# Kernel optimization log

Measured on AMD Instinct MI355X. Metric: run time of the kernel, lower is better.

Reference implementation:

```python
import jax, jax.numpy as jnp
import numpy as np

B, S, E, H = 4, 2048, 1024, 16
D = E // H  # head_dim = 64
SCALE = D ** -0.5
NEG_INF = -1e9


def setup_inputs() -> dict:
    key = jax.random.key(0)
    ks = jax.random.split(key, 12)
    p = 1.0 / np.sqrt(E)  # nn.Linear default init scale
    inp = {
        'query': jax.random.normal(ks[0], (B, S, E), jnp.float32),
        'key': jax.random.normal(ks[1], (B, S, E), jnp.float32),
        'value': jax.random.normal(ks[2], (B, S, E), jnp.float32),
        'mask': jnp.ones((B, S, S), jnp.int32),
        'Wq': jax.random.uniform(ks[3], (E, E), jnp.float32, -p, p),
        'bq': jax.random.uniform(ks[4], (E,), jnp.float32, -p, p),
        'Wk': jax.random.uniform(ks[5], (E, E), jnp.float32, -p, p),
        'bk': jax.random.uniform(ks[6], (E,), jnp.float32, -p, p),
        'Wv': jax.random.uniform(ks[7], (E, E), jnp.float32, -p, p),
        'bv': jax.random.uniform(ks[8], (E,), jnp.float32, -p, p),
        'Wo': jax.random.uniform(ks[9], (E, E), jnp.float32, -p, p),
        'bo': jax.random.uniform(ks[10], (E,), jnp.float32, -p, p),
    }
    return inp


def _heads(x):
    # [B, S, E] -> [B, H, S, D]
    b, s, _ = x.shape
    return x.reshape(b, s, H, D).transpose(0, 2, 1, 3)


def reference(query, key, value, mask, Wq, bq, Wk, bk, Wv, bv, Wo, bo):
    # separate QKV projections (nn.Linear: x @ W.T + b)
    q = _heads(query @ Wq.T + bq) * SCALE  # query pre-scaled as in module
    k = _heads(key @ Wk.T + bk)
    v = _heads(value @ Wv.T + bv)
    # scaled dot-product attention with explicit score matrix
    scores = jnp.einsum('bhqd,bhkd->bhqk', q, k)  # [B, H, S, S]
    m = mask[:, None, :, :]  # broadcast over heads
    scores = jnp.where(m == 0, NEG_INF, scores)
    attn = jax.nn.softmax(scores, axis=-1)
    out = jnp.einsum('bhqk,bhkd->bhqd', attn, v)  # [B, H, S, D]
    out = out.transpose(0, 2, 1, 3).reshape(query.shape[0], -1, E)
    return out @ Wo.T + bo
```

## Files before the change

### kernel.cpp

```cpp
#include <hip/hip_runtime.h>


#define B_ 4
#define S_ 2048
#define E_ 1024
#define H_ 16
#define D_ 64

typedef __attribute__((ext_vector_type(4))) float f32x4;
typedef __attribute__((ext_vector_type(8))) short short8;
typedef __attribute__((ext_vector_type(4))) short short4v;
typedef __attribute__((ext_vector_type(8))) __bf16 bf16x8;
typedef __attribute__((ext_vector_type(4))) __bf16 bf16x4;
typedef unsigned short u16;
typedef unsigned int u32;

#define MFMA16(A, Bf, C) __builtin_amdgcn_mfma_f32_16x16x32_bf16((A), (Bf), (C), 0, 0, 0)

#define FMAXB2 12.0f

__device__ __forceinline__ f32x4 mfma_pv(short4v a, short4v b, f32x4 c) {
  return __builtin_amdgcn_mfma_f32_16x16x16bf16_1k(a, b, c, 0, 0, 0);
}

__device__ __forceinline__ u16 f2bf(float f) {
  u32 u = __float_as_uint(f);
  u += 0x7FFFu + ((u >> 16) & 1u);
  return (u16)(u >> 16);
}

__device__ __forceinline__ void async16(const void* g, void* l) {
  __builtin_amdgcn_global_load_lds((const __attribute__((address_space(1))) u32*)g,
                                   (__attribute__((address_space(3))) u32*)l, 16, 0, 0);
}

__device__ __forceinline__ short4v packp(float a, float b, float c, float d) {
  bf16x4 t;
  t[0] = (__bf16)a; t[1] = (__bf16)b; t[2] = (__bf16)c; t[3] = (__bf16)d;
  return __builtin_bit_cast(short4v, t);
}

__device__ __forceinline__ float exp2fast(float x) {
  return __builtin_amdgcn_exp2f(x);
}

__global__ __launch_bounds__(256) void cvt8_kernel(const float* __restrict__ a0,
                                                   const float* __restrict__ a1,
                                                   const float* __restrict__ a2,
                                                   const float* __restrict__ w0,
                                                   const float* __restrict__ w1,
                                                   const float* __restrict__ w2,
                                                   const float* __restrict__ w3,
                                                   u16* __restrict__ da0,
                                                   u16* __restrict__ da1,
                                                   u16* __restrict__ da2,
                                                   u16* __restrict__ dw0,
                                                   u16* __restrict__ dw1,
                                                   u16* __restrict__ dw2,
                                                   u16* __restrict__ dw3,
                                                   const int* __restrict__ mask,
                                                   u32* __restrict__ mbits,
                                                   int* __restrict__ rowOK,
                                                   int n4a, int n4w) {
  int z = blockIdx.y;
  if (z == 7) {
    if (blockIdx.x >= 2048) return;
    int w = threadIdx.x >> 6, t = threadIdx.x & 63;
    int row = blockIdx.x * 4 + w;
    const int4* p = (const int4*)(mask + (size_t)row * S_ + t * 32);
    u32 bits = 0;
#pragma unroll
    for (int i = 0; i < 8; ++i) {
      int4 v = p[i];
      bits |= (v.x != 0 ? 1u : 0u) << (i * 4 + 0);
      bits |= (v.y != 0 ? 1u : 0u) << (i * 4 + 1);
      bits |= (v.z != 0 ? 1u : 0u) << (i * 4 + 2);
      bits |= (v.w != 0 ? 1u : 0u) << (i * 4 + 3);
    }
    mbits[(size_t)row * 64 + t] = bits;
    unsigned long long all1 = __ballot(bits == 0xFFFFFFFFu);
    if (t == 0) rowOK[row] = (all1 == 0xFFFFFFFFFFFFFFFFull) ? 1 : 0;
    return;
  }
  const float* src;
  u16* dst;
  int n4;
  switch (z) {
    case 0: src = a0; dst = da0; n4 = n4a; break;
    case 1: src = a1; dst = da1; n4 = n4a; break;
    case 2: src = a2; dst = da2; n4 = n4a; break;
    case 3: src = w0; dst = dw0; n4 = n4w; break;
    case 4: src = w1; dst = dw1; n4 = n4w; break;
    case 5: src = w2; dst = dw2; n4 = n4w; break;
    default: src = w3; dst = dw3; n4 = n4w; break;
  }
  int i = blockIdx.x * 256 + threadIdx.x;
  if (i >= n4) return;
  float4 v = ((const float4*)src)[i];
  short4v o;
  o[0] = (short)f2bf(v.x); o[1] = (short)f2bf(v.y);
  o[2] = (short)f2bf(v.z); o[3] = (short)f2bf(v.w);
  ((short4v*)dst)[i] = o;
}

__device__ __forceinline__ void gemm_swizzle(int* m0, int* n0) {
  int s = blockIdx.y * 8 + blockIdx.x;
  int L = (s & 7) * 64 + (s >> 3);
  *m0 = (L >> 3) * 128;
  *n0 = (L & 7) * 128;
}

__device__ __forceinline__ void gemm_mainloop_128(const u16* __restrict__ A,
                                                  const u16* __restrict__ W,
                                                  int m0, int n0,
                                                  u16* As, u16* Bs,
                                                  f32x4 acc[4][4], int tid) {
  int w = tid >> 6, l = tid & 63, lo = l & 15, g = l >> 4;
  int wm = w >> 1, wn = w & 1;
  int srow = w * 32 + (l >> 3);
  int scol = ((l & 7) ^ (l >> 3)) * 8;
  const u16* ga0 = A + (size_t)(m0 + srow) * E_ + scol;
  const u16* gb0 = W + (size_t)(n0 + srow) * E_ + scol;
  char* la0 = (char*)As + w * 4096;
  char* lb0 = (char*)Bs + w * 4096;

  for (int k0 = 0; k0 < E_; k0 += 64) {
#pragma unroll
    for (int i = 0; i < 4; ++i) {
      async16(ga0 + (size_t)i * 8 * E_ + k0, la0 + i * 1024);
      async16(gb0 + (size_t)i * 8 * E_ + k0, lb0 + i * 1024);
    }
    __syncthreads();
#pragma unroll
    for (int kh = 0; kh < 2; ++kh) {
      bf16x8 af[4], bf[4];
#pragma unroll
      for (int mi = 0; mi < 4; ++mi) {
        int r = wm * 64 + mi * 16 + lo;
        af[mi] = *(const bf16x8*)((char*)As + r * 128 + (((kh * 4 + g) ^ (r & 7)) * 16));
      }
#pragma unroll
      for (int ni = 0; ni < 4; ++ni) {
        int r = wn * 64 + ni * 16 + lo;
        bf[ni] = *(const bf16x8*)((char*)Bs + r * 128 + (((kh * 4 + g) ^ (r & 7)) * 16));
      }
#pragma unroll
      for (int mi = 0; mi < 4; ++mi)
#pragma unroll
        for (int ni = 0; ni < 4; ++ni)
          acc[mi][ni] = MFMA16(af[mi], bf[ni], acc[mi][ni]);
    }
    __syncthreads();
  }
}

__global__ __launch_bounds__(256) void gemm_qkv_kernel(
    const u16* __restrict__ qin, const u16* __restrict__ kin, const u16* __restrict__ vin,
    const u16* __restrict__ wq, const u16* __restrict__ wk, const u16* __restrict__ wv,
    const float* __restrict__ bq, const float* __restrict__ bk, const float* __restrict__ bv,
    u16* __restrict__ Qo, u16* __restrict__ Ko, u16* __restrict__ Vo) {
  __shared__ u16 As[128 * 64];
  __shared__ u16 Bs[128 * 64];
  int z = blockIdx.z;
  const u16* A = z == 0 ? qin : (z == 1 ? kin : vin);
  const u16* W = z == 0 ? wq : (z == 1 ? wk : wv);
  const float* bias = z == 0 ? bq : (z == 1 ? bk : bv);
  u16* O = z == 0 ? Qo : (z == 1 ? Ko : Vo);
  float scale = z == 0 ? 0.125f * 1.44269504f : 1.0f;
  int m0, n0;
  gemm_swizzle(&m0, &n0);
  f32x4 acc[4][4];
#pragma unroll
  for (int mi = 0; mi < 4; ++mi)
#pragma unroll
    for (int ni = 0; ni < 4; ++ni) acc[mi][ni] = (f32x4){0.f, 0.f, 0.f, 0.f};
  int tid = threadIdx.x;
  gemm_mainloop_128(A, W, m0, n0, As, Bs, acc, tid);
  int w = tid >> 6, l = tid & 63, lo = l & 15, g = l >> 4;
  int wm = w >> 1, wn = w & 1;
#pragma unroll
  for (int mi = 0; mi < 4; ++mi)
#pragma unroll
    for (int ni = 0; ni < 4; ++ni) {
      int n = n0 + wn * 64 + ni * 16 + lo;
      int h = n >> 6, d = n & 63;
      float bb = bias[n];
      int mbase = m0 + wm * 64 + mi * 16 + g * 4;
      int b = mbase >> 11, s = mbase & 2047;
      if (z == 2) {
        short4v ov;
#pragma unroll
        for (int j = 0; j < 4; ++j) ov[j] = (short)f2bf(acc[mi][ni][j] + bb);
        *(short4v*)(O + (((size_t)(b * H_ + h)) * D_ + d) * S_ + s) = ov;
      } else {
#pragma unroll
        for (int j = 0; j < 4; ++j) {
          float val = (acc[mi][ni][j] + bb) * scale;
          O[(((size_t)(b * H_ + h)) * S_ + (s + j)) * D_ + d] = f2bf(val);
        }
      }
    }
}

__global__ __launch_bounds__(256) void gemm_out_kernel(const u16* __restrict__ A,
                                                       const u16* __restrict__ W,
                                                       const float* __restrict__ bias,
                                                       float* __restrict__ O) {
  __shared__ u16 As[128 * 64];
  __shared__ u16 Bs[128 * 64];
  int m0, n0;
  gemm_swizzle(&m0, &n0);
  f32x4 acc[4][4];
#pragma unroll
  for (int mi = 0; mi < 4; ++mi)
#pragma unroll
    for (int ni = 0; ni < 4; ++ni) acc[mi][ni] = (f32x4){0.f, 0.f, 0.f, 0.f};
  int tid = threadIdx.x;
  gemm_mainloop_128(A, W, m0, n0, As, Bs, acc, tid);
  int w = tid >> 6, l = tid & 63, lo = l & 15, g = l >> 4;
  int wm = w >> 1, wn = w & 1;
#pragma unroll
  for (int mi = 0; mi < 4; ++mi)
#pragma unroll
    for (int ni = 0; ni < 4; ++ni) {
      int n = n0 + wn * 64 + ni * 16 + lo;
      float bb = bias[n];
#pragma unroll
      for (int j = 0; j < 4; ++j) {
        int m = m0 + wm * 64 + mi * 16 + g * 4 + j;
        O[(size_t)m * E_ + n] = acc[mi][ni][j] + bb;
      }
    }
}

__global__ __launch_bounds__(256) void attn_kernel(const u16* __restrict__ Q,
                                                   const u16* __restrict__ K,
                                                   const u16* __restrict__ VT,
                                                   u16* __restrict__ AO,
                                                   const u32* __restrict__ mbits,
                                                   const int* __restrict__ rowOK) {
  __shared__ u16 Kt0[4096], Kt1[4096];
  __shared__ u16 Vt0[4096], Vt1[4096];
  __shared__ int s_ok;

  int tid = threadIdx.x;
  int w = tid >> 6, l = tid & 63, lo = l & 15, g = l >> 4;
  int flat = blockIdx.y * gridDim.x + blockIdx.x;
  int L = (flat & 7) * 128 + (flat >> 3);
  int bh = L >> 4;
  int b = bh >> 4, h = bh & 15;
  int q0 = (L & 15) * 128;

  if (tid == 0) s_ok = 1;
  __syncthreads();
  if (tid < 128 && rowOK[b * S_ + q0 + tid] == 0) s_ok = 0;
  __syncthreads();
  const bool use_mask = (s_ok == 0);

  const u16* Qb = Q + (size_t)bh * S_ * D_;
  const u16* Kb = K + (size_t)bh * S_ * D_;
  const u16* VTb = VT + (size_t)bh * D_ * S_;

  const u16* kg[2];
  const u16* vgb[2];
  int lbase[2];
#pragma unroll
  for (int r = 0; r < 2; ++r) {
    int kb = r * 4 + w;
    int tr = kb * 8 + (l >> 3);
    int dc = (l & 7) ^ (l >> 3);
    kg[r] = Kb + (size_t)tr * D_ + dc * 8;
    vgb[r] = VTb + (size_t)tr * S_ + dc * 8;
    lbase[r] = kb * 512;
  }
#pragma unroll
  for (int r = 0; r < 2; ++r) {
    async16(kg[r], &Kt0[lbase[r]]);
    async16(vgb[r], &Vt0[lbase[r]]);
  }

  int qrow = q0 + w * 32;
  bf16x8 qf[2][2];
#pragma unroll
  for (int qi = 0; qi < 2; ++qi)
#pragma unroll
    for (int kc = 0; kc < 2; ++kc)
      qf[qi][kc] = *(const bf16x8*)(Qb + (size_t)(qrow + qi * 16 + lo) * D_ + kc * 32 + g * 8);

  f32x4 ot[4][2];
  f32x4 lacc[2];
#pragma unroll
  for (int di = 0; di < 4; ++di)
#pragma unroll
    for (int qi = 0; qi < 2; ++qi) ot[di][qi] = (f32x4){0.f, 0.f, 0.f, 0.f};
  lacc[0] = (f32x4){0.f, 0.f, 0.f, 0.f};
  lacc[1] = (f32x4){0.f, 0.f, 0.f, 0.f};
  float m_run[2] = {-__builtin_inff(), -__builtin_inff()};
  const short4v onesv = {(short)0x3F80, (short)0x3F80, (short)0x3F80, (short)0x3F80};
  const f32x4 cinit = {-FMAXB2, -FMAXB2, -FMAXB2, -FMAXB2};

  auto tile_body = [&](const u16* KtC, const u16* VtC, u16* KtN, u16* VtN, int kk) {
    __syncthreads();
    if (kk + 64 < S_) {
#pragma unroll
      for (int r = 0; r < 2; ++r) {
        async16(kg[r] + (size_t)(kk + 64) * D_, &KtN[lbase[r]]);
        async16(vgb[r] + (kk + 64), &VtN[lbase[r]]);
      }
    }
    const char* Ktc = (const char*)KtC;
    const char* Vtc = (const char*)VtC;

    short4v pb[4][2];
    if (!use_mask) {
      __builtin_amdgcn_s_setprio(1);
#pragma unroll
      for (int ks = 0; ks < 4; ++ks) {
        int row = ks * 16 + lo;
        bf16x8 a0 = *(const bf16x8*)(Ktc + row * 128 + ((g * 16) ^ ((row & 7) << 4)));
        bf16x8 a1 = *(const bf16x8*)(Ktc + row * 128 + ((64 + g * 16) ^ ((row & 7) << 4)));
        f32x4 c0 = MFMA16(a0, qf[0][0], cinit);
        c0 = MFMA16(a1, qf[0][1], c0);
        f32x4 c1 = MFMA16(a0, qf[1][0], cinit);
        c1 = MFMA16(a1, qf[1][1], c1);
        pb[ks][0] = packp(exp2fast(c0[0]), exp2fast(c0[1]), exp2fast(c0[2]),
                          exp2fast(c0[3]));
        pb[ks][1] = packp(exp2fast(c1[0]), exp2fast(c1[1]), exp2fast(c1[2]),
                          exp2fast(c1[3]));
      }
      __builtin_amdgcn_s_setprio(0);
    } else {
      float tmx[2] = {-__builtin_inff(), -__builtin_inff()};
#pragma unroll
      for (int ks = 0; ks < 4; ++ks) {
        int row = ks * 16 + lo;
        bf16x8 a0 = *(const bf16x8*)(Ktc + row * 128 + ((g * 16) ^ ((row & 7) << 4)));
        bf16x8 a1 = *(const bf16x8*)(Ktc + row * 128 + ((64 + g * 16) ^ ((row & 7) << 4)));
#pragma unroll
        for (int qi = 0; qi < 2; ++qi) {
          f32x4 c = MFMA16(a0, qf[qi][0], cinit);
          c = MFMA16(a1, qf[qi][1], c);
          int q = qrow + qi * 16 + lo;
          u32 word = mbits[((size_t)(b * S_ + q)) * 64 + ((kk + ks * 16 + g * 4) >> 5)];
#pragma unroll
          for (int j = 0; j < 4; ++j) {
            int kkk = ks * 16 + g * 4 + j;
            if (!((word >> ((kk + kkk) & 31)) & 1u)) c[j] = -1e9f;
            tmx[qi] = fmaxf(tmx[qi], c[j]);
          }
        }
      }
#pragma unroll
      for (int qi = 0; qi < 2; ++qi) {
        float t = tmx[qi];
        t = fmaxf(t, __shfl_xor(t, 16, 64));
        t = fmaxf(t, __shfl_xor(t, 32, 64));
        float mnew = fmaxf(m_run[qi], t);
        float alpha = exp2fast(m_run[qi] - mnew);
        m_run[qi] = mnew;
#pragma unroll
        for (int di = 0; di < 4; ++di) ot[di][qi] *= alpha;
        lacc[qi] *= alpha;
      }
#pragma unroll
      for (int ks = 0; ks < 4; ++ks) {
        int row = ks * 16 + lo;
        bf16x8 a0 = *(const bf16x8*)(Ktc + row * 128 + ((g * 16) ^ ((row & 7) << 4)));
        bf16x8 a1 = *(const bf16x8*)(Ktc + row * 128 + ((64 + g * 16) ^ ((row & 7) << 4)));
#pragma unroll
        for (int qi = 0; qi < 2; ++qi) {
          f32x4 c = MFMA16(a0, qf[qi][0], cinit);
          c = MFMA16(a1, qf[qi][1], c);
          int q = qrow + qi * 16 + lo;
          u32 word = mbits[((size_t)(b * S_ + q)) * 64 + ((kk + ks * 16 + g * 4) >> 5)];
          float mm = m_run[qi];
#pragma unroll
          for (int j = 0; j < 4; ++j) {
            int kkk = ks * 16 + g * 4 + j;
            if (!((word >> ((kk + kkk) & 31)) & 1u)) c[j] = -1e9f;
            c[j] = exp2fast(c[j] - mm);
          }
          pb[ks][qi] = packp(c[0], c[1], c[2], c[3]);
        }
      }
    }

#pragma unroll
    for (int ks = 0; ks < 4; ++ks)
#pragma unroll
      for (int qi = 0; qi < 2; ++qi)
        lacc[qi] = mfma_pv(onesv, pb[ks][qi], lacc[qi]);

    short4v vaA[4], vaB[4];
#define LOADVA(arr, ksv)                                                              \
  _Pragma("unroll") for (int di = 0; di < 4; ++di) {                                  \
    int r = di * 16 + lo;                                                             \
    int chunk = (ksv)*2 + (g >> 1);                                                   \
    arr[di] = *(const short4v*)(Vtc + r * 128 + (((chunk * 16) ^ ((r & 7) << 4))) +   \
                                ((g & 1) * 8));                                       \
  }
#define MFMAKS(arr, ksv)                                                              \
  _Pragma("unroll") for (int qi = 0; qi < 2; ++qi) {                                  \
    _Pragma("unroll") for (int di = 0; di < 4; ++di)                                  \
        ot[di][qi] = mfma_pv(arr[di], pb[ksv][qi], ot[di][qi]);                       \
  }
    LOADVA(vaA, 0)
    LOADVA(vaB, 1)
    __builtin_amdgcn_s_setprio(1);
    MFMAKS(vaA, 0)
    LOADVA(vaA, 2)
    MFMAKS(vaB, 1)
    LOADVA(vaB, 3)
    MFMAKS(vaA, 2)
    MFMAKS(vaB, 3)
    __builtin_amdgcn_s_setprio(0);
#undef LOADVA
#undef MFMAKS
  };

  for (int k0 = 0; k0 < S_; k0 += 128) {
    tile_body(Kt0, Vt0, Kt1, Vt1, k0);
    tile_body(Kt1, Vt1, Kt0, Vt0, k0 + 64);
  }

#pragma unroll
  for (int qi = 0; qi < 2; ++qi) {
    float inv = 1.f / lacc[qi][0];
    int q = qrow + qi * 16 + lo;
#pragma unroll
    for (int di = 0; di < 4; ++di) {
      f32x4 o = ot[di][qi] * inv;
      short4v ov = packp(o[0], o[1], o[2], o[3]);
      *(short4v*)(AO + ((size_t)(b * S_ + q)) * E_ + h * 64 + di * 16 + g * 4) = ov;
    }
  }
}

extern "C" void kernel_launch(void* const* d_in, const int* in_sizes, int n_in,
                              void* d_out, int out_size, void* d_ws, size_t ws_size,
                              hipStream_t stream) {
  const float* query = (const float*)d_in[0];
  const float* key   = (const float*)d_in[1];
  const float* value = (const float*)d_in[2];
  const int*   mask  = (const int*)d_in[3];
  const float* Wq = (const float*)d_in[4];
  const float* bq = (const float*)d_in[5];
  const float* Wk = (const float*)d_in[6];
  const float* bk = (const float*)d_in[7];
  const float* Wv = (const float*)d_in[8];
  const float* bv = (const float*)d_in[9];
  const float* Wo = (const float*)d_in[10];
  const float* bo = (const float*)d_in[11];
  float* out = (float*)d_out;

  char* ws = (char*)d_ws;
  size_t off = 0;
  auto alloc = [&](size_t bytes) -> char* {
    char* p = ws + off;
    off += (bytes + 255) & ~(size_t)255;
    return p;
  };
  const size_t ACT = (size_t)8192 * 1024 * 2;
  const size_t WMT = (size_t)1024 * 1024 * 2;
  u16* qbf = (u16*)alloc(ACT);
  u16* kbf = (u16*)alloc(ACT);
  u16* vbf = (u16*)alloc(ACT);
  u16* wqb = (u16*)alloc(WMT);
  u16* wkb = (u16*)alloc(WMT);
  u16* wvb = (u16*)alloc(WMT);
  u16* wob = (u16*)alloc(WMT);
  u16* Qd = (u16*)alloc(ACT);
  u16* Kd = (u16*)alloc(ACT);
  u16* VTd = (u16*)alloc(ACT);
  u16* AO = (u16*)alloc(ACT);
  u32* mb = (u32*)alloc((size_t)B_ * S_ * 64 * 4);
  int* rOK = (int*)alloc((size_t)B_ * S_ * 4);
  (void)in_sizes; (void)n_in; (void)out_size; (void)ws_size;

  int n4a = B_ * S_ * E_ / 4;
  int n4w = E_ * E_ / 4;
  cvt8_kernel<<<dim3((n4a + 255) / 256, 8), 256, 0, stream>>>(
      query, key, value, Wq, Wk, Wv, Wo, qbf, kbf, vbf, wqb, wkb, wvb, wob, mask, mb, rOK,
      n4a, n4w);
  gemm_qkv_kernel<<<dim3(8, 64, 3), 256, 0, stream>>>(
      qbf, kbf, vbf, wqb, wkb, wvb, bq, bk, bv, Qd, Kd, VTd);
  attn_kernel<<<dim3(16, 64), 256, 0, stream>>>(Qd, Kd, VTd, AO, mb, rOK);
  gemm_out_kernel<<<dim3(8, 64), 256, 0, stream>>>(AO, wob, bo, out);
}
```

Baseline: 233.3 us.

## Double-buffer GEMM shared-memory tiles and use 8 waves per block

The projection GEMMs now use two LDS buffers for A and B, so the async global-to-LDS copy of the next K slice is issued before the MFMA work on the current slice. Blocks grow to 512 threads (8 waves), and each wave computes a 32x64 sub-tile instead of 64x64, which reduces per-wave accumulator registers. The aim is to hide global load latency and raise occupancy. The costs are doubled LDS per block, fewer MFMAs per LDS fragment load, and a synchronisation pattern that depends on the async copies having completed at each barrier.

```diff
diff --git a/kernel.cpp b/kernel.cpp
--- a/kernel.cpp
+++ b/kernel.cpp
@@ -113,54 +113,59 @@
 __device__ __forceinline__ void gemm_mainloop_128(const u16* __restrict__ A,
                                                   const u16* __restrict__ W,
                                                   int m0, int n0,
-                                                  u16* As, u16* Bs,
-                                                  f32x4 acc[4][4], int tid) {
-  int w = tid >> 6, l = tid & 63, lo = l & 15, g = l >> 4;
+                                                  u16* As0, u16* As1, u16* Bs0, u16* Bs1,
+                                                  f32x4 acc[2][4], int tid) {
+  int w = tid >> 6, l = tid & 63, lo = l & 15, g = (l >> 4) & 3;
   int wm = w >> 1, wn = w & 1;
-  int srow = w * 32 + (l >> 3);
+  int srow = w * 16 + (l >> 3);
   int scol = ((l & 7) ^ (l >> 3)) * 8;
   const u16* ga0 = A + (size_t)(m0 + srow) * E_ + scol;
   const u16* gb0 = W + (size_t)(n0 + srow) * E_ + scol;
-  char* la0 = (char*)As + w * 4096;
-  char* lb0 = (char*)Bs + w * 4096;
-
-  for (int k0 = 0; k0 < E_; k0 += 64) {
-#pragma unroll
-    for (int i = 0; i < 4; ++i) {
-      async16(ga0 + (size_t)i * 8 * E_ + k0, la0 + i * 1024);
-      async16(gb0 + (size_t)i * 8 * E_ + k0, lb0 + i * 1024);
-    }
+  int ldst = w * 2048;
+
+#define STAGE_(As, Bs, k0)                                                       \
+  _Pragma("unroll") for (int i = 0; i < 2; ++i) {                                \
+    async16(ga0 + (size_t)i * 8 * E_ + (k0), (char*)(As) + ldst + i * 1024);     \
+    async16(gb0 + (size_t)i * 8 * E_ + (k0), (char*)(Bs) + ldst + i * 1024);     \
+  }
+#define COMPUTE_(As, Bs)                                                         \
+  _Pragma("unroll") for (int kh = 0; kh < 2; ++kh) {                             \
+    bf16x8 af[2], bf[4];                                                         \
+    _Pragma("unroll") for (int mi = 0; mi < 2; ++mi) {                           \
+      int r = wm * 32 + mi * 16 + lo;                                            \
+      af[mi] = *(const bf16x8*)((const char*)(As) + r * 128 +                    \
+                                (((kh * 4 + g) ^ (r & 7)) * 16));                \
+    }                                                                            \
+    _Pragma("unroll") for (int ni = 0; ni < 4; ++ni) {                           \
+      int r = wn * 64 + ni * 16 + lo;                                            \
+      bf[ni] = *(const bf16x8*)((const char*)(Bs) + r * 128 +                    \
+                                (((kh * 4 + g) ^ (r & 7)) * 16));                \
+    }                                                                            \
+    _Pragma("unroll") for (int mi = 0; mi < 2; ++mi)                             \
+      _Pragma("unroll") for (int ni = 0; ni < 4; ++ni)                           \
+          acc[mi][ni] = MFMA16(af[mi], bf[ni], acc[mi][ni]);                     \
+  }
+
+  STAGE_(As0, Bs0, 0)
+  for (int k0 = 0; k0 < E_; k0 += 128) {
     __syncthreads();
-#pragma unroll
-    for (int kh = 0; kh < 2; ++kh) {
-      bf16x8 af[4], bf[4];
-#pragma unroll
-      for (int mi = 0; mi < 4; ++mi) {
-        int r = wm * 64 + mi * 16 + lo;
-        af[mi] = *(const bf16x8*)((char*)As + r * 128 + (((kh * 4 + g) ^ (r & 7)) * 16));
-      }
-#pragma unroll
-      for (int ni = 0; ni < 4; ++ni) {
-        int r = wn * 64 + ni * 16 + lo;
-        bf[ni] = *(const bf16x8*)((char*)Bs + r * 128 + (((kh * 4 + g) ^ (r & 7)) * 16));
-      }
-#pragma unroll
-      for (int mi = 0; mi < 4; ++mi)
-#pragma unroll
-        for (int ni = 0; ni < 4; ++ni)
-          acc[mi][ni] = MFMA16(af[mi], bf[ni], acc[mi][ni]);
-    }
+    STAGE_(As1, Bs1, k0 + 64)
+    COMPUTE_(As0, Bs0)
     __syncthreads();
-  }
-}
-
-__global__ __launch_bounds__(256) void gemm_qkv_kernel(
+    if (k0 + 128 < E_) { STAGE_(As0, Bs0, k0 + 128) }
+    COMPUTE_(As1, Bs1)
+  }
+#undef STAGE_
+#undef COMPUTE_
+}
+
+__global__ __launch_bounds__(512) void gemm_qkv_kernel(
     const u16* __restrict__ qin, const u16* __restrict__ kin, const u16* __restrict__ vin,
     const u16* __restrict__ wq, const u16* __restrict__ wk, const u16* __restrict__ wv,
     const float* __restrict__ bq, const float* __restrict__ bk, const float* __restrict__ bv,
     u16* __restrict__ Qo, u16* __restrict__ Ko, u16* __restrict__ Vo) {
-  __shared__ u16 As[128 * 64];
-  __shared__ u16 Bs[128 * 64];
+  __shared__ u16 As0[128 * 64], As1[128 * 64];
+  __shared__ u16 Bs0[128 * 64], Bs1[128 * 64];
   int z = blockIdx.z;
   const u16* A = z == 0 ? qin : (z == 1 ? kin : vin);
   const u16* W = z == 0 ? wq : (z == 1 ? wk : wv);
@@ -169,23 +174,23 @@
   float scale = z == 0 ? 0.125f * 1.44269504f : 1.0f;
   int m0, n0;
   gemm_swizzle(&m0, &n0);
-  f32x4 acc[4][4];
-#pragma unroll
-  for (int mi = 0; mi < 4; ++mi)
+  f32x4 acc[2][4];
+#pragma unroll
+  for (int mi = 0; mi < 2; ++mi)
 #pragma unroll
     for (int ni = 0; ni < 4; ++ni) acc[mi][ni] = (f32x4){0.f, 0.f, 0.f, 0.f};
   int tid = threadIdx.x;
-  gemm_mainloop_128(A, W, m0, n0, As, Bs, acc, tid);
-  int w = tid >> 6, l = tid & 63, lo = l & 15, g = l >> 4;
+  gemm_mainloop_128(A, W, m0, n0, As0, As1, Bs0, Bs1, acc, tid);
+  int w = tid >> 6, l = tid & 63, lo = l & 15, g = (l >> 4) & 3;
   int wm = w >> 1, wn = w & 1;
 #pragma unroll
-  for (int mi = 0; mi < 4; ++mi)
+  for (int mi = 0; mi < 2; ++mi)
 #pragma unroll
     for (int ni = 0; ni < 4; ++ni) {
       int n = n0 + wn * 64 + ni * 16 + lo;
       int h = n >> 6, d = n & 63;
       float bb = bias[n];
-      int mbase = m0 + wm * 64 + mi * 16 + g * 4;
+      int mbase = m0 + wm * 32 + mi * 16 + g * 4;
       int b = mbase >> 11, s = mbase & 2047;
       if (z == 2) {
         short4v ov;
@@ -202,32 +207,32 @@
     }
 }
 
-__global__ __launch_bounds__(256) void gemm_out_kernel(const u16* __restrict__ A,
+__global__ __launch_bounds__(512) void gemm_out_kernel(const u16* __restrict__ A,
                                                        const u16* __restrict__ W,
                                                        const float* __restrict__ bias,
                                                        float* __restrict__ O) {
-  __shared__ u16 As[128 * 64];
-  __shared__ u16 Bs[128 * 64];
+  __shared__ u16 As0[128 * 64], As1[128 * 64];
+  __shared__ u16 Bs0[128 * 64], Bs1[128 * 64];
   int m0, n0;
   gemm_swizzle(&m0, &n0);
-  f32x4 acc[4][4];
-#pragma unroll
-  for (int mi = 0; mi < 4; ++mi)
+  f32x4 acc[2][4];
+#pragma unroll
+  for (int mi = 0; mi < 2; ++mi)
 #pragma unroll
     for (int ni = 0; ni < 4; ++ni) acc[mi][ni] = (f32x4){0.f, 0.f, 0.f, 0.f};
   int tid = threadIdx.x;
-  gemm_mainloop_128(A, W, m0, n0, As, Bs, acc, tid);
-  int w = tid >> 6, l = tid & 63, lo = l & 15, g = l >> 4;
+  gemm_mainloop_128(A, W, m0, n0, As0, As1, Bs0, Bs1, acc, tid);
+  int w = tid >> 6, l = tid & 63, lo = l & 15, g = (l >> 4) & 3;
   int wm = w >> 1, wn = w & 1;
 #pragma unroll
-  for (int mi = 0; mi < 4; ++mi)
+  for (int mi = 0; mi < 2; ++mi)
 #pragma unroll
     for (int ni = 0; ni < 4; ++ni) {
       int n = n0 + wn * 64 + ni * 16 + lo;
       float bb = bias[n];
 #pragma unroll
       for (int j = 0; j < 4; ++j) {
-        int m = m0 + wm * 64 + mi * 16 + g * 4 + j;
+        int m = m0 + wm * 32 + mi * 16 + g * 4 + j;
         O[(size_t)m * E_ + n] = acc[mi][ni][j] + bb;
       }
     }
@@ -482,8 +487,8 @@
   cvt8_kernel<<<dim3((n4a + 255) / 256, 8), 256, 0, stream>>>(
       query, key, value, Wq, Wk, Wv, Wo, qbf, kbf, vbf, wqb, wkb, wvb, wob, mask, mb, rOK,
       n4a, n4w);
-  gemm_qkv_kernel<<<dim3(8, 64, 3), 256, 0, stream>>>(
+  gemm_qkv_kernel<<<dim3(8, 64, 3), 512, 0, stream>>>(
       qbf, kbf, vbf, wqb, wkb, wvb, bq, bk, bv, Qd, Kd, VTd);
   attn_kernel<<<dim3(16, 64), 256, 0, stream>>>(Qd, Kd, VTd, AO, mb, rOK);
-  gemm_out_kernel<<<dim3(8, 64), 256, 0, stream>>>(AO, wob, bo, out);
-}
+  gemm_out_kernel<<<dim3(8, 64), 512, 0, stream>>>(AO, wob, bo, out);
+}
```

Result: no change. 232.7 us (-0.3%).
